# Performance work log

Hardware: AMD Instinct MI355X
Metric: run time of the kernel (lower is better)

Reference implementation:

```python
import jax, jax.numpy as jnp
import numpy as np

N, C_IN, C_OUT, T, V, S = 32, 64, 64, 512, 25, 3
R = C_IN // 2  # rel_channels (in_channel not in (3,9) -> in//rel_reduction=2)
EPS = 1e-5


def setup_inputs() -> dict:
    key = jax.random.key(0)
    ks = jax.random.split(key, 14)
    p = lambda k, shape, s=0.05: jax.random.normal(k, shape, dtype=jnp.float32) * s
    return {
        "x": jax.random.normal(ks[0], (N, C_IN, T, V), dtype=jnp.float32),
        "A": p(ks[1], (S, V, V), 0.2),            # fixed adjacency per subset
        "w1": p(ks[2], (S, R, C_IN)),             # conv1 1x1 per subset
        "b1": p(ks[3], (S, R)),
        "w2": p(ks[4], (S, R, C_IN)),             # conv2 1x1
        "b2": p(ks[5], (S, R)),
        "w3": p(ks[6], (S, C_OUT, C_IN)),         # conv3 1x1 (value)
        "b3": p(ks[7], (S, C_OUT)),
        "w4": p(ks[8], (S, C_OUT, R)),            # conv4 1x1 on relation tensor
        "b4": p(ks[9], (S, C_OUT)),
        "alpha": p(ks[10], (S,), 0.1),            # per-subset scalar (nn.Parameter zeros(1); randomized for non-degenerate test)
        "bn_gamma": jnp.ones((C_OUT,), dtype=jnp.float32),
        "bn_beta": jnp.zeros((C_OUT,), dtype=jnp.float32),
    }


def reference(x, A, w1, b1, w2, b2, w3, b3, w4, b4, alpha, bn_gamma, bn_beta):
    # x: [N,C,T,V]. 1x1 conv commutes with mean over T, so pool first (same math).
    xm = x.mean(axis=2)                                              # [N,C,V]
    q = jnp.einsum('ncv,src->nsrv', xm, w1) + b1[None, :, :, None]   # conv1(x).mean(-2)
    k = jnp.einsum('ncv,src->nsrv', xm, w2) + b2[None, :, :, None]   # conv2(x).mean(-2)
    v = jnp.einsum('nctv,soc->nsotv', x, w3) + b3[None, :, :, None, None]  # conv3(x)
    # outer difference over nodes: [N,S,R,V,V]
    rel = jax.nn.relu(q[..., :, None] - k[..., None, :])
    # conv4 (1x1 over rel channels) * alpha + A[s]
    att = jnp.einsum('nsruv,sor->nsouv', rel, w4) + b4[None, :, :, None, None]
    att = att * alpha[None, :, None, None, None] + A[None, :, None, :, :]  # [N,S,O,V,V]
    # aggregation: einsum('ncuv,nctv->nctu') summed over subsets
    y = jnp.einsum('nsouv,nsotv->notu', att, v)                      # [N,O,T,V]
    # BatchNorm2d in training mode (batch statistics, biased variance)
    mu = y.mean(axis=(0, 2, 3), keepdims=True)
    var = y.var(axis=(0, 2, 3), keepdims=True)
    ybn = (y - mu) * jax.lax.rsqrt(var + EPS) * bn_gamma[None, :, None, None] + bn_beta[None, :, None, None]
    # act(y) + bn(y) + residual (Identity since in_channel == out_channel)
    return jax.nn.relu(y) + ybn + x
```

## Files before the change

### kernel.cpp

```cpp
#include <hip/hip_runtime.h>
#include <hip/hip_bf16.h>

#define XM_OFF   0
#define SSUM_OFF 51200
#define SSQ_OFF  51264
#define SCL_OFF  51328
#define SHF_OFF  51392
#define ATTF_BYTE_OFF (51456ull * 4ull)
#define Y_BYTE_OFF (ATTF_BYTE_OFF + 12582912ull)

typedef __attribute__((ext_vector_type(8))) short short8;
typedef __attribute__((ext_vector_type(4))) float f32x4;

__device__ __forceinline__ ushort f2bs(float f) {
  __hip_bfloat16 h = __float2bfloat16(f);
  ushort u; __builtin_memcpy(&u, &h, 2); return u;
}
__device__ __forceinline__ float bs2f(ushort u) {
  return __uint_as_float((unsigned)u << 16);
}

__global__ __launch_bounds__(256) void k_xm(const float* __restrict__ x,
                                            float* __restrict__ ws) {
  const int b = blockIdx.x;
  const int tid = threadIdx.x;
  if (b == 0 && tid < 128) ws[SSUM_OFF + tid] = 0.f;
  const float* base = x + (size_t)b * 12800;
  float acc[25];
#pragma unroll
  for (int v = 0; v < 25; ++v) acc[v] = 0.f;
  for (int t = tid; t < 512; t += 256) {
    const float* row = base + t * 25;
#pragma unroll
    for (int v = 0; v < 25; ++v) acc[v] += row[v];
  }
  __shared__ float red[256][25];
#pragma unroll
  for (int v = 0; v < 25; ++v) red[tid][v] = acc[v];
  __syncthreads();
  for (int st = 128; st > 0; st >>= 1) {
    if (tid < st) {
#pragma unroll
      for (int v = 0; v < 25; ++v) red[tid][v] += red[tid + st][v];
    }
    __syncthreads();
  }
  if (tid < 25) ws[XM_OFF + b * 25 + tid] = red[0][tid] * (1.0f / 512.0f);
}

__global__ __launch_bounds__(256) void k_att(const float* __restrict__ ws,
    const float* __restrict__ A, const float* __restrict__ w1, const float* __restrict__ b1,
    const float* __restrict__ w2, const float* __restrict__ b2, const float* __restrict__ w4,
    const float* __restrict__ b4, const float* __restrict__ alpha, uint* __restrict__ attf) {
  const int b = blockIdx.x;
  const int n = b / 24; const int r = b % 24; const int s = r >> 3; const int og = r & 7;
  const int tid = threadIdx.x;
  __shared__ float xs[1600];
  __shared__ float qb[800];
  __shared__ float kb[800];
  __shared__ float att8[8][625];
  for (int j = tid; j < 1600; j += 256) xs[j] = ws[XM_OFF + n * 1600 + j];
  __syncthreads();
  for (int i = tid; i < 1600; i += 256) {
    const int half = i / 800;
    const int ii = i % 800;
    const int rr = ii / 25, v = ii % 25;
    const float* w = half ? w2 : w1;
    const float* bb = half ? b2 : b1;
    float acc = bb[s * 32 + rr];
    const float* wr = w + (s * 32 + rr) * 64;
#pragma unroll 8
    for (int c = 0; c < 64; ++c) acc += wr[c] * xs[c * 25 + v];
    (half ? kb : qb)[ii] = acc;
  }
  __syncthreads();
  const float al = alpha[s];
  for (int i = tid; i < 5000; i += 256) {
    const int o2 = i / 625, r2 = i % 625;
    const int u = r2 / 25, v = r2 % 25;
    const int o = og * 8 + o2;
    const float* wr = w4 + (s * 64 + o) * 32;
    float acc = 0.f;
#pragma unroll 8
    for (int rr2 = 0; rr2 < 32; ++rr2) {
      const float d = qb[rr2 * 25 + u] - kb[rr2 * 25 + v];
      acc += wr[rr2] * fmaxf(d, 0.f);
    }
    att8[o2][r2] = (acc + b4[s * 64 + o]) * al + A[s * 625 + r2];
  }
  __syncthreads();
  for (int w = tid; w < 4096; w += 256) {
    const int o2 = w >> 9, widx = w & 511;
    const int mt = widx >> 8, lane = (widx >> 2) & 63, pr = widx & 3;
    const int kg = lane >> 4, colu = lane & 15;
    const int u = mt * 16 + colu;
    const int i0 = pr * 2;
    const int v0 = kg * 4 + (i0 & 3) + ((i0 >> 2) << 4);
    const float f0 = (u < 25 && v0 < 25) ? att8[o2][u * 25 + v0] : 0.f;
    const float f1 = (u < 25 && (v0 + 1) < 25) ? att8[o2][u * 25 + v0 + 1] : 0.f;
    attf[((size_t)(n * 3 + s) * 64 + og * 8 + o2) * 512 + widx] =
        (uint)f2bs(f0) | ((uint)f2bs(f1) << 16);
  }
}

__global__ __launch_bounds__(512, 2) void k_fused(const float* __restrict__ x,
    const float* __restrict__ w3, const float* __restrict__ b3,
    const ushort* __restrict__ attf, float* __restrict__ ssum, float* __restrict__ ssq,
    ushort* __restrict__ yg) {
  __shared__ ushort xl[64 * 404];
  __shared__ ushort vs[64 * 400];
  __shared__ float sS[64], sQ[64];
  const int bid = blockIdx.x;
  const int xcd = bid & 7, jj = bid >> 3;
  const int n = xcd + ((jj >> 5) << 3);
  const int tc = jj & 31;
  const int t0 = tc << 4;
  const int tid = threadIdx.x;
  const int lane = tid & 63, wid = tid >> 6;
  const int kg = lane >> 4, col = lane & 15;

  {
    const float* xb = x + (size_t)n * 819200 + t0 * 25;
    for (int i = tid; i < 6400; i += 512) {
      const int c = i / 100, r = i - c * 100;
      const float4 f = *(const float4*)(xb + (size_t)c * 12800 + (r << 2));
      ushort4 p; p.x = f2bs(f.x); p.y = f2bs(f.y); p.z = f2bs(f.z); p.w = f2bs(f.w);
      *(ushort4*)&xl[c * 404 + (r << 2)] = p;
    }
  }

  f32x4 yacc[8][2];
#pragma unroll
  for (int oi = 0; oi < 8; ++oi) { yacc[oi][0] = (f32x4)0.f; yacc[oi][1] = (f32x4)0.f; }

  __syncthreads();

  const int od = wid << 3;

  for (int s = 0; s < 3; ++s) {
    short8 af[4][2];
    float4 b3f[4];
#pragma unroll
    for (int mt = 0; mt < 4; ++mt) {
      const float* wrow = w3 + ((size_t)s * 64 + mt * 16 + col) * 64;
#pragma unroll
      for (int kb = 0; kb < 2; ++kb) {
        const float4 lo = *(const float4*)(wrow + kb * 32 + kg * 4);
        const float4 hi = *(const float4*)(wrow + kb * 32 + 16 + kg * 4);
        short8 a;
        a[0] = (short)f2bs(lo.x); a[1] = (short)f2bs(lo.y);
        a[2] = (short)f2bs(lo.z); a[3] = (short)f2bs(lo.w);
        a[4] = (short)f2bs(hi.x); a[5] = (short)f2bs(hi.y);
        a[6] = (short)f2bs(hi.z); a[7] = (short)f2bs(hi.w);
        af[mt][kb] = a;
      }
      b3f[mt] = *(const float4*)(b3 + s * 64 + mt * 16 + kg * 4);
    }

    for (int nt = wid; nt < 25; nt += 8) {
      const int item = nt * 16 + col;
      short8 b0, b1;
#pragma unroll
      for (int i = 0; i < 8; ++i) {
        const int c0 = kg * 4 + (i & 3) + ((i >> 2) << 4);
        b0[i] = (short)xl[c0 * 404 + item];
        b1[i] = (short)xl[(c0 + 32) * 404 + item];
      }
#pragma unroll
      for (int mt = 0; mt < 4; ++mt) {
        f32x4 acc;
        acc[0] = b3f[mt].x; acc[1] = b3f[mt].y; acc[2] = b3f[mt].z; acc[3] = b3f[mt].w;
        acc = __builtin_amdgcn_mfma_f32_16x16x32_bf16(af[mt][0], b0, acc, 0, 0, 0);
        acc = __builtin_amdgcn_mfma_f32_16x16x32_bf16(af[mt][1], b1, acc, 0, 0, 0);
#pragma unroll
        for (int r = 0; r < 4; ++r)
          vs[(mt * 16 + kg * 4 + r) * 400 + item] = f2bs(acc[r]);
      }
    }
    __syncthreads();

    const ushort* apbase = attf + (((size_t)(n * 3 + s) * 64 + od) << 10);
#pragma unroll
    for (int oi = 0; oi < 8; ++oi) {
      const ushort* ap = apbase + ((size_t)oi << 10);
      const short8 A0 = *(const short8*)(ap + lane * 8);
      const short8 A1 = *(const short8*)(ap + 512 + lane * 8);
      short8 bfr;
#pragma unroll
      for (int i = 0; i < 8; ++i) {
        const int v = kg * 4 + (i & 3) + ((i >> 2) << 4);
        bfr[i] = (v < 25) ? (short)vs[(od + oi) * 400 + col * 25 + v] : (short)0;
      }
      yacc[oi][0] = __builtin_amdgcn_mfma_f32_16x16x32_bf16(A0, bfr, yacc[oi][0], 0, 0, 0);
      yacc[oi][1] = __builtin_amdgcn_mfma_f32_16x16x32_bf16(A1, bfr, yacc[oi][1], 0, 0, 0);
    }
    __syncthreads();
  }

#pragma unroll
  for (int oi = 0; oi < 8; ++oi) {
    float a1 = 0.f, a2 = 0.f;
#pragma unroll
    for (int mt = 0; mt < 2; ++mt) {
#pragma unroll
      for (int r = 0; r < 4; ++r) {
        const int u = mt * 16 + kg * 4 + r;
        if (u < 25) {
          const float v = yacc[oi][mt][r];
          a1 += v; a2 += v * v;
        }
      }
    }
#pragma unroll
    for (int off = 32; off > 0; off >>= 1) {
      a1 += __shfl_down(a1, off);
      a2 += __shfl_down(a2, off);
    }
    if (lane == 0) { sS[od + oi] = a1; sQ[od + oi] = a2; }
  }

#pragma unroll
  for (int oi = 0; oi < 8; ++oi) {
#pragma unroll
    for (int mt = 0; mt < 2; ++mt) {
      const int u0 = mt * 16 + kg * 4;
#pragma unroll
      for (int r = 0; r < 4; ++r) {
        const int u = u0 + r;
        if (u < 25) vs[(od + oi) * 400 + col * 25 + u] = f2bs(yacc[oi][mt][r]);
      }
    }
  }
  __syncthreads();

  {
    const size_t ybase = ((size_t)n * 64) * 12800 + (size_t)t0 * 25;
    for (int k2 = tid; k2 < 3200; k2 += 512) {
      const int o = k2 / 50, rem = k2 - o * 50;
      const int4 w = *(const int4*)&vs[o * 400 + rem * 8];
      *(int4*)(yg + ybase + (size_t)o * 12800 + rem * 8) = w;
    }
  }
  if (tid < 64) {
    atomicAdd(&ssum[tid], sS[tid]);
    atomicAdd(&ssq[tid], sQ[tid]);
  }
}

__global__ __launch_bounds__(64) void k_stats(const float* __restrict__ ssum,
    const float* __restrict__ ssq, const float* __restrict__ gamma,
    const float* __restrict__ beta, float* __restrict__ scl, float* __restrict__ shf) {
  const int o = threadIdx.x;
  const float inv = 1.0f / 409600.0f;
  const float mu = ssum[o] * inv;
  const float var = ssq[o] * inv - mu * mu;
  const float rstd = rsqrtf(var + 1e-5f);
  const float sc = gamma[o] * rstd;
  scl[o] = sc;
  shf[o] = beta[o] - mu * sc;
}

__global__ __launch_bounds__(256) void k_final(const float* __restrict__ x,
    const ushort* __restrict__ yg, const float* __restrict__ scl,
    const float* __restrict__ shf, float* __restrict__ out) {
  const int stride = gridDim.x * blockDim.x;
  for (int i = blockIdx.x * 256 + threadIdx.x; i < 6553600; i += stride) {
    const int o = (i / 3200) & 63;
    const float sc = scl[o], sh = shf[o];
    const float4 xv = ((const float4*)x)[i];
    const ushort4 yu = ((const ushort4*)yg)[i];
    const float y0 = bs2f(yu.x), y1 = bs2f(yu.y), y2 = bs2f(yu.z), y3 = bs2f(yu.w);
    float4 r;
    r.x = fmaxf(y0, 0.f) + y0 * sc + sh + xv.x;
    r.y = fmaxf(y1, 0.f) + y1 * sc + sh + xv.y;
    r.z = fmaxf(y2, 0.f) + y2 * sc + sh + xv.z;
    r.w = fmaxf(y3, 0.f) + y3 * sc + sh + xv.w;
    ((float4*)out)[i] = r;
  }
}

extern "C" void kernel_launch(void* const* d_in, const int* in_sizes, int n_in,
                              void* d_out, int out_size, void* d_ws, size_t ws_size,
                              hipStream_t stream) {
  const float* x     = (const float*)d_in[0];
  const float* A     = (const float*)d_in[1];
  const float* w1    = (const float*)d_in[2];
  const float* b1    = (const float*)d_in[3];
  const float* w2    = (const float*)d_in[4];
  const float* b2    = (const float*)d_in[5];
  const float* w3    = (const float*)d_in[6];
  const float* b3    = (const float*)d_in[7];
  const float* w4    = (const float*)d_in[8];
  const float* b4    = (const float*)d_in[9];
  const float* alpha = (const float*)d_in[10];
  const float* gamma = (const float*)d_in[11];
  const float* beta  = (const float*)d_in[12];
  float* ws = (float*)d_ws;
  uint* attf_w = (uint*)((char*)d_ws + ATTF_BYTE_OFF);
  const ushort* attf_r = (const ushort*)((char*)d_ws + ATTF_BYTE_OFF);
  ushort* yg = (ushort*)((char*)d_ws + Y_BYTE_OFF);
  float* out = (float*)d_out;

  k_xm<<<2048, 256, 0, stream>>>(x, ws);
  k_att<<<768, 256, 0, stream>>>(ws, A, w1, b1, w2, b2, w4, b4, alpha, attf_w);
  k_fused<<<1024, 512, 0, stream>>>(x, w3, b3, attf_r, ws + SSUM_OFF, ws + SSQ_OFF, yg);
  k_stats<<<1, 64, 0, stream>>>(ws + SSUM_OFF, ws + SSQ_OFF, gamma, beta,
                                ws + SCL_OFF, ws + SHF_OFF);
  k_final<<<2048, 256, 0, stream>>>(x, yg, ws + SCL_OFF, ws + SHF_OFF, out);
}
```

Before: 414.8 us.

## Split fused kernel over output-channel halves, prepack w3 and relayout LDS tiles

The fused conv3+aggregation kernel is split so each block handles half of the 64 output channels, which doubles the grid to 2048 blocks and cuts LDS use so more blocks fit per CU (launch bounds 512,4). w3 is converted to bf16 MFMA fragments once in a new small kernel instead of in every block. x and v tiles in LDS get new layouts so MFMA operands come from vector loads and paired stores. Per-wave atomics replace the block-level stat reduction. Each block still loads and converts the full 64-channel x tile, so x reads and the conv3 MFMA input staging are duplicated across the two halves, and the number of atomics grows.

```diff
diff --git a/kernel.cpp b/kernel.cpp
--- a/kernel.cpp
+++ b/kernel.cpp
@@ -6,8 +6,9 @@
 #define SSQ_OFF  51264
 #define SCL_OFF  51328
 #define SHF_OFF  51392
-#define ATTF_BYTE_OFF (51456ull * 4ull)
-#define Y_BYTE_OFF (ATTF_BYTE_OFF + 12582912ull)
+#define W3F_BYTE_OFF  (51456ull * 4ull)
+#define ATTF_BYTE_OFF (W3F_BYTE_OFF + 24576ull)
+#define Y_BYTE_OFF    (ATTF_BYTE_OFF + 12582912ull)
 
 typedef __attribute__((ext_vector_type(8))) short short8;
 typedef __attribute__((ext_vector_type(4))) float f32x4;
@@ -103,93 +104,114 @@
   }
 }
 
-__global__ __launch_bounds__(512, 2) void k_fused(const float* __restrict__ x,
-    const float* __restrict__ w3, const float* __restrict__ b3,
+__global__ __launch_bounds__(512) void k_wpack(const float* __restrict__ w3,
+                                               short8* __restrict__ w3f) {
+  const int s = blockIdx.x;
+  const int tid = threadIdx.x;
+  const int mt = tid >> 7, kb2 = (tid >> 6) & 1, lane = tid & 63;
+  const int kg = lane >> 4, col = lane & 15;
+  const int o = mt * 16 + col;
+  const float* wrow = w3 + ((size_t)s * 64 + o) * 64;
+  const float4 lo = *(const float4*)(wrow + kb2 * 32 + kg * 4);
+  const float4 hi = *(const float4*)(wrow + kb2 * 32 + 16 + kg * 4);
+  short8 a;
+  a[0] = (short)f2bs(lo.x); a[1] = (short)f2bs(lo.y);
+  a[2] = (short)f2bs(lo.z); a[3] = (short)f2bs(lo.w);
+  a[4] = (short)f2bs(hi.x); a[5] = (short)f2bs(hi.y);
+  a[6] = (short)f2bs(hi.z); a[7] = (short)f2bs(hi.w);
+  w3f[((s * 4 + mt) * 2 + kb2) * 64 + lane] = a;
+}
+
+__global__ __launch_bounds__(512, 4) void k_fused(const float* __restrict__ x,
+    const short8* __restrict__ w3f, const float* __restrict__ b3,
     const ushort* __restrict__ attf, float* __restrict__ ssum, float* __restrict__ ssq,
     ushort* __restrict__ yg) {
-  __shared__ ushort xl[64 * 404];
-  __shared__ ushort vs[64 * 400];
-  __shared__ float sS[64], sQ[64];
+  __shared__ ushort xl[2][25][64][8];
+  __shared__ ushort vs[15232];
   const int bid = blockIdx.x;
-  const int xcd = bid & 7, jj = bid >> 3;
-  const int n = xcd + ((jj >> 5) << 3);
-  const int tc = jj & 31;
+  const int xcd = bid & 7, j = bid >> 3;
+  const int n = xcd * 4 + (j >> 6);
+  const int r0 = j & 63;
+  const int tc = r0 >> 1, oh = r0 & 1;
   const int t0 = tc << 4;
   const int tid = threadIdx.x;
   const int lane = tid & 63, wid = tid >> 6;
   const int kg = lane >> 4, col = lane & 15;
 
   {
-    const float* xb = x + (size_t)n * 819200 + t0 * 25;
-    for (int i = tid; i < 6400; i += 512) {
-      const int c = i / 100, r = i - c * 100;
-      const float4 f = *(const float4*)(xb + (size_t)c * 12800 + (r << 2));
-      ushort4 p; p.x = f2bs(f.x); p.y = f2bs(f.y); p.z = f2bs(f.z); p.w = f2bs(f.w);
-      *(ushort4*)&xl[c * 404 + (r << 2)] = p;
-    }
-  }
-
-  f32x4 yacc[8][2];
-#pragma unroll
-  for (int oi = 0; oi < 8; ++oi) { yacc[oi][0] = (f32x4)0.f; yacc[oi][1] = (f32x4)0.f; }
-
-  __syncthreads();
-
-  const int od = wid << 3;
+    uint* vz = (uint*)vs;
+    for (int i = tid; i < 7616; i += 512) vz[i] = 0u;
+  }
+  if (tid < 400) {
+    const float* xb = x + (size_t)n * 819200 + t0 * 25 + tid;
+    const int scol = tid & 15, snt = tid >> 4;
+#pragma unroll
+    for (int cq = 0; cq < 16; ++cq) {
+      const int c0 = cq * 4;
+      const float f0 = xb[(size_t)(c0 + 0) * 12800];
+      const float f1 = xb[(size_t)(c0 + 1) * 12800];
+      const float f2 = xb[(size_t)(c0 + 2) * 12800];
+      const float f3 = xb[(size_t)(c0 + 3) * 12800];
+      ushort4 p;
+      p.x = f2bs(f0); p.y = f2bs(f1); p.z = f2bs(f2); p.w = f2bs(f3);
+      *(ushort4*)&xl[c0 >> 5][snt][(cq & 3) * 16 + scol][((c0 >> 4) & 1) * 4] = p;
+    }
+  }
+
+  f32x4 yacc[4][2];
+#pragma unroll
+  for (int oi = 0; oi < 4; ++oi) { yacc[oi][0] = (f32x4)0.f; yacc[oi][1] = (f32x4)0.f; }
+
+  const int od_l = wid << 2;
+  const int og0 = oh << 5;
+
+  __syncthreads();
 
   for (int s = 0; s < 3; ++s) {
-    short8 af[4][2];
-    float4 b3f[4];
-#pragma unroll
-    for (int mt = 0; mt < 4; ++mt) {
-      const float* wrow = w3 + ((size_t)s * 64 + mt * 16 + col) * 64;
-#pragma unroll
-      for (int kb = 0; kb < 2; ++kb) {
-        const float4 lo = *(const float4*)(wrow + kb * 32 + kg * 4);
-        const float4 hi = *(const float4*)(wrow + kb * 32 + 16 + kg * 4);
-        short8 a;
-        a[0] = (short)f2bs(lo.x); a[1] = (short)f2bs(lo.y);
-        a[2] = (short)f2bs(lo.z); a[3] = (short)f2bs(lo.w);
-        a[4] = (short)f2bs(hi.x); a[5] = (short)f2bs(hi.y);
-        a[6] = (short)f2bs(hi.z); a[7] = (short)f2bs(hi.w);
-        af[mt][kb] = a;
-      }
-      b3f[mt] = *(const float4*)(b3 + s * 64 + mt * 16 + kg * 4);
+    short8 af[2][2];
+    float4 b3f[2];
+#pragma unroll
+    for (int mt = 0; mt < 2; ++mt) {
+      const int mt_abs = (oh << 1) + mt;
+#pragma unroll
+      for (int kb2 = 0; kb2 < 2; ++kb2)
+        af[mt][kb2] = w3f[((s * 4 + mt_abs) * 2 + kb2) * 64 + lane];
+      b3f[mt] = *(const float4*)(b3 + s * 64 + og0 + mt * 16 + kg * 4);
     }
 
     for (int nt = wid; nt < 25; nt += 8) {
+      const short8 bf0 = *(const short8*)&xl[0][nt][lane][0];
+      const short8 bf1 = *(const short8*)&xl[1][nt][lane][0];
       const int item = nt * 16 + col;
-      short8 b0, b1;
-#pragma unroll
-      for (int i = 0; i < 8; ++i) {
-        const int c0 = kg * 4 + (i & 3) + ((i >> 2) << 4);
-        b0[i] = (short)xl[c0 * 404 + item];
-        b1[i] = (short)xl[(c0 + 32) * 404 + item];
-      }
-#pragma unroll
-      for (int mt = 0; mt < 4; ++mt) {
+      const int t = item / 25;
+      const int v = item - t * 25;
+      const int vsbase = (t * 28 + v) * 34;
+#pragma unroll
+      for (int mt = 0; mt < 2; ++mt) {
         f32x4 acc;
         acc[0] = b3f[mt].x; acc[1] = b3f[mt].y; acc[2] = b3f[mt].z; acc[3] = b3f[mt].w;
-        acc = __builtin_amdgcn_mfma_f32_16x16x32_bf16(af[mt][0], b0, acc, 0, 0, 0);
-        acc = __builtin_amdgcn_mfma_f32_16x16x32_bf16(af[mt][1], b1, acc, 0, 0, 0);
-#pragma unroll
-        for (int r = 0; r < 4; ++r)
-          vs[(mt * 16 + kg * 4 + r) * 400 + item] = f2bs(acc[r]);
+        acc = __builtin_amdgcn_mfma_f32_16x16x32_bf16(af[mt][0], bf0, acc, 0, 0, 0);
+        acc = __builtin_amdgcn_mfma_f32_16x16x32_bf16(af[mt][1], bf1, acc, 0, 0, 0);
+        uint* dst = (uint*)&vs[vsbase + mt * 16 + kg * 4];
+        dst[0] = (uint)f2bs(acc[0]) | ((uint)f2bs(acc[1]) << 16);
+        dst[1] = (uint)f2bs(acc[2]) | ((uint)f2bs(acc[3]) << 16);
       }
     }
     __syncthreads();
 
-    const ushort* apbase = attf + (((size_t)(n * 3 + s) * 64 + od) << 10);
-#pragma unroll
-    for (int oi = 0; oi < 8; ++oi) {
-      const ushort* ap = apbase + ((size_t)oi << 10);
+    const ushort* apb = attf + (((size_t)(n * 3 + s) * 64 + og0 + od_l) << 10);
+#pragma unroll
+    for (int oi = 0; oi < 4; ++oi) {
+      const ushort* ap = apb + ((size_t)oi << 10);
       const short8 A0 = *(const short8*)(ap + lane * 8);
       const short8 A1 = *(const short8*)(ap + 512 + lane * 8);
+      const int o_l = od_l + oi;
       short8 bfr;
 #pragma unroll
       for (int i = 0; i < 8; ++i) {
-        const int v = kg * 4 + (i & 3) + ((i >> 2) << 4);
-        bfr[i] = (v < 25) ? (short)vs[(od + oi) * 400 + col * 25 + v] : (short)0;
+        int v = kg * 4 + (i & 3) + ((i >> 2) << 4);
+        v = (v < 28) ? v : 27;
+        bfr[i] = (short)vs[(col * 28 + v) * 34 + o_l];
       }
       yacc[oi][0] = __builtin_amdgcn_mfma_f32_16x16x32_bf16(A0, bfr, yacc[oi][0], 0, 0, 0);
       yacc[oi][1] = __builtin_amdgcn_mfma_f32_16x16x32_bf16(A1, bfr, yacc[oi][1], 0, 0, 0);
@@ -198,16 +220,16 @@
   }
 
 #pragma unroll
-  for (int oi = 0; oi < 8; ++oi) {
+  for (int oi = 0; oi < 4; ++oi) {
     float a1 = 0.f, a2 = 0.f;
 #pragma unroll
     for (int mt = 0; mt < 2; ++mt) {
 #pragma unroll
-      for (int r = 0; r < 4; ++r) {
-        const int u = mt * 16 + kg * 4 + r;
+      for (int r2 = 0; r2 < 4; ++r2) {
+        const int u = mt * 16 + kg * 4 + r2;
         if (u < 25) {
-          const float v = yacc[oi][mt][r];
-          a1 += v; a2 += v * v;
+          const float vv = yacc[oi][mt][r2];
+          a1 += vv; a2 += vv * vv;
         }
       }
     }
@@ -216,34 +238,31 @@
       a1 += __shfl_down(a1, off);
       a2 += __shfl_down(a2, off);
     }
-    if (lane == 0) { sS[od + oi] = a1; sQ[od + oi] = a2; }
-  }
-
-#pragma unroll
-  for (int oi = 0; oi < 8; ++oi) {
+    if (lane == 0) {
+      atomicAdd(&ssum[og0 + od_l + oi], a1);
+      atomicAdd(&ssq[og0 + od_l + oi], a2);
+    }
+  }
+
+#pragma unroll
+  for (int oi = 0; oi < 4; ++oi) {
+    const int o_l = od_l + oi;
 #pragma unroll
     for (int mt = 0; mt < 2; ++mt) {
-      const int u0 = mt * 16 + kg * 4;
-#pragma unroll
-      for (int r = 0; r < 4; ++r) {
-        const int u = u0 + r;
-        if (u < 25) vs[(od + oi) * 400 + col * 25 + u] = f2bs(yacc[oi][mt][r]);
+#pragma unroll
+      for (int r2 = 0; r2 < 4; ++r2) {
+        const int u = mt * 16 + kg * 4 + r2;
+        if (u < 25) vs[o_l * 408 + col * 25 + u] = f2bs(yacc[oi][mt][r2]);
       }
     }
   }
   __syncthreads();
-
   {
-    const size_t ybase = ((size_t)n * 64) * 12800 + (size_t)t0 * 25;
-    for (int k2 = tid; k2 < 3200; k2 += 512) {
+    const size_t ybase = ((size_t)n * 64 + og0) * 12800 + (size_t)t0 * 25;
+    for (int k2 = tid; k2 < 1600; k2 += 512) {
       const int o = k2 / 50, rem = k2 - o * 50;
-      const int4 w = *(const int4*)&vs[o * 400 + rem * 8];
-      *(int4*)(yg + ybase + (size_t)o * 12800 + rem * 8) = w;
-    }
-  }
-  if (tid < 64) {
-    atomicAdd(&ssum[tid], sS[tid]);
-    atomicAdd(&ssq[tid], sQ[tid]);
+      *(int4*)(yg + ybase + (size_t)o * 12800 + rem * 8) = *(const int4*)&vs[o * 408 + rem * 8];
+    }
   }
 }
 
@@ -296,6 +315,7 @@
   const float* gamma = (const float*)d_in[11];
   const float* beta  = (const float*)d_in[12];
   float* ws = (float*)d_ws;
+  short8* w3f = (short8*)((char*)d_ws + W3F_BYTE_OFF);
   uint* attf_w = (uint*)((char*)d_ws + ATTF_BYTE_OFF);
   const ushort* attf_r = (const ushort*)((char*)d_ws + ATTF_BYTE_OFF);
   ushort* yg = (ushort*)((char*)d_ws + Y_BYTE_OFF);
@@ -303,7 +323,8 @@
 
   k_xm<<<2048, 256, 0, stream>>>(x, ws);
   k_att<<<768, 256, 0, stream>>>(ws, A, w1, b1, w2, b2, w4, b4, alpha, attf_w);
-  k_fused<<<1024, 512, 0, stream>>>(x, w3, b3, attf_r, ws + SSUM_OFF, ws + SSQ_OFF, yg);
+  k_wpack<<<3, 512, 0, stream>>>(w3, w3f);
+  k_fused<<<2048, 512, 0, stream>>>(x, w3f, b3, attf_r, ws + SSUM_OFF, ws + SSQ_OFF, yg);
   k_stats<<<1, 64, 0, stream>>>(ws + SSUM_OFF, ws + SSQ_OFF, gamma, beta,
                                 ws + SCL_OFF, ws + SHF_OFF);
   k_final<<<2048, 256, 0, stream>>>(x, yg, ws + SCL_OFF, ws + SHF_OFF, out);
```

After: 688.2 us. 65.9% more time.
